# Kernel tuning notes

Hardware: AMD Instinct MI355X
Metric: run time of the kernel (lower is better)

## Reference

```python
import jax, jax.numpy as jnp
import numpy as np

NEG_SLOPE = 0.1  # negative slope of LeakyReLU in Conv3dReLU/Conv2dReLU


def setup_inputs() -> dict:
    key = jax.random.key(0)
    ks = jax.random.split(key, 16)
    B, C, PREV, N, M1, M2 = 2, 16, 16, 16384, 4096, 4096
    D1, CORR, FILT = 4, 15, 15          # d1 = d+1; (r+1)^d1 - r^d1 with r=1
    CO0, CO1 = 32, 32                    # num_corr_output
    O0, O1 = 64, 64                      # num_output
    CIN = 2 * C + PREV                   # corr_conv input channels

    feat1 = jax.random.normal(ks[0], (B, C, M1), jnp.float32)
    feat2 = jax.random.normal(ks[1], (B, C, M2), jnp.float32)
    prev_corr_feat = jax.random.normal(ks[2], (B, PREV, N), jnp.float32)
    barycentric1 = jax.random.uniform(ks[3], (B, D1, N), jnp.float32)
    # lattice_offset1: batch-offset flattened indices into [0, B*(M1+1)); value -1+1=0 is the pad slot
    local = jax.random.randint(ks[4], (B, D1, N), 0, M1)
    lattice_offset1 = local + (jnp.arange(B, dtype=jnp.int64) * (M1 + 1))[:, None, None]
    pc1_corr_indices = jax.random.randint(ks[5], (B, CORR, M1), -1, M1).astype(jnp.int64)
    pc2_corr_indices = jax.random.randint(ks[6], (B, FILT, CORR, M1), -1, M2).astype(jnp.int64)

    s = 0.05
    cw0 = jax.random.normal(ks[7], (CO0, CIN, CORR), jnp.float32) * s   # Conv3d (1,corr_size,1)
    cb0 = jax.random.normal(ks[8], (CO0,), jnp.float32) * s
    cw1 = jax.random.normal(ks[9], (CO1, CO0), jnp.float32) * s        # Conv3d 1x1x1
    cb1 = jax.random.normal(ks[10], (CO1,), jnp.float32) * s
    bw0 = jax.random.normal(ks[11], (O0, CO1, FILT), jnp.float32) * s  # Conv2d (filter_size,1)
    bb0 = jax.random.normal(ks[12], (O0,), jnp.float32) * s
    bw1 = jax.random.normal(ks[13], (O1, O0), jnp.float32) * s         # Conv2d 1x1 (no relu)
    bb1 = jax.random.normal(ks[14], (O1,), jnp.float32) * s

    return {
        "feat1": feat1, "feat2": feat2, "prev_corr_feat": prev_corr_feat,
        "barycentric1": barycentric1,
        "cw0": cw0, "cb0": cb0, "cw1": cw1, "cb1": cb1,
        "bw0": bw0, "bb0": bb0, "bw1": bw1, "bb1": bb1,
        "lattice_offset1": lattice_offset1,
        "pc1_corr_indices": pc1_corr_indices,
        "pc2_corr_indices": pc2_corr_indices,
        "max_hash_cnt1": M1, "max_hash_cnt2": M2,
    }


def reference(feat1, feat2, prev_corr_feat, barycentric1,
              cw0, cb0, cw1, cb1, bw0, bb0, bw1, bb1,
              lattice_offset1, pc1_corr_indices, pc2_corr_indices,
              max_hash_cnt1, max_hash_cnt2):
    B, C, M1 = feat1.shape
    PREV = prev_corr_feat.shape[1]

    # ---- splat prev_corr_feat onto lattice vertices (scatter-add) ----
    flat_idx = (lattice_offset1 + 1).reshape(-1)                      # (B*d1*N,)
    # (B, PREV, d1, N) -> (B, d1, N, PREV) -> (B*d1*N, PREV)
    vals = (barycentric1[:, None, :, :] * prev_corr_feat[:, :, None, :])
    vals = vals.transpose(0, 2, 3, 1).reshape(-1, PREV)
    prev_splat = jax.ops.segment_sum(vals, flat_idx, num_segments=B * (M1 + 1))
    prev_splat = prev_splat.reshape(B, M1 + 1, PREV).transpose(0, 2, 1)  # (B, PREV, M1+1)

    # use_norm: normalize by splatted barycentric mass
    ones_splat = jax.ops.segment_sum(barycentric1.reshape(-1), flat_idx,
                                     num_segments=B * (M1 + 1)).reshape(B, M1 + 1)
    prev_splat = prev_splat * (1.0 / (ones_splat + 1e-5))[:, None, :]

    # ---- prepend zero pad slot (index 0 catches -1 neighbor indices) ----
    splat1 = jnp.concatenate([prev_splat, jnp.pad(feat1, ((0, 0), (0, 0), (1, 0)))], axis=1)  # (B, PREV+C, M1+1)
    splat2 = jnp.pad(feat2, ((0, 0), (0, 0), (1, 0)))                                          # (B, C, M2+1)

    # ---- irregular gathers ----
    g1 = jax.vmap(lambda s, i: s[:, i])(splat1, pc1_corr_indices + 1)   # (B, PREV+C, corr, M1)
    g2 = jax.vmap(lambda s, i: s[:, i])(splat2, pc2_corr_indices + 1)   # (B, C, filt, corr, M1)
    FILT = g2.shape[2]
    g1b = jnp.broadcast_to(g1[:, :, None], (B, g1.shape[1], FILT, g1.shape[2], M1))
    combined = jnp.concatenate([g1b, g2], axis=1)                       # (B, 2C+PREV, filt, corr, M1)

    # ---- corr_conv: Conv3d(1,corr,1)+LeakyReLU, then 1x1x1+LeakyReLU ----
    x = jnp.einsum('bifkn,oik->bofn', combined, cw0) + cb0[None, :, None, None]
    x = jax.nn.leaky_relu(x, NEG_SLOPE)
    x = jnp.einsum('bcfn,oc->bofn', x, cw1) + cb1[None, :, None, None]
    x = jax.nn.leaky_relu(x, NEG_SLOPE)

    # ---- blur_conv: Conv2d(filt,1)+LeakyReLU, then 1x1 (last_relu=False) ----
    y = jnp.einsum('bcfn,ocf->bon', x, bw0) + bb0[None, :, None]
    y = jax.nn.leaky_relu(y, NEG_SLOPE)
    y = jnp.einsum('bcn,oc->bon', y, bw1) + bb1[None, :, None]
    return y
```

## Files before the change

### kernel.cpp

```cpp
#include <hip/hip_runtime.h>
#include <hip/hip_bf16.h>

namespace {

constexpr int B     = 2;
constexpr int C     = 16;
constexpr int PREVC = 16;
constexpr int NPTS  = 16384;
constexpr int M1    = 4096;
constexpr int D1    = 4;
constexpr int CORR  = 15;
constexpr int FILT  = 15;
constexpr int CIN   = 48;
constexpr int CO0   = 32;
constexpr int O1    = 64;
constexpr int MS    = M1 + 1;
constexpr int NSLOT = B * MS;
constexpr int NPAIR = B * D1 * NPTS;
constexpr int BCAP  = 64;
constexpr int GSTR  = 240;
constexpr float NEG = 0.1f;

constexpr size_t OFF_SP1   = 0;
constexpr size_t SZ_SP1    = (size_t)NSLOT * 32;
constexpr size_t OFF_SP2   = OFF_SP1 + SZ_SP1;
constexpr size_t SZ_SP2    = (size_t)NSLOT * 16;
constexpr size_t OFF_P     = OFF_SP2 + SZ_SP2;
constexpr size_t SZ_PQ     = (size_t)B * CORR * MS * 32 / 2;
constexpr size_t OFF_Q     = OFF_P + SZ_PQ;
constexpr size_t OFF_CWT   = OFF_Q + SZ_PQ;
constexpr size_t SZ_CWT    = (size_t)CORR * CIN * 32;
constexpr size_t OFF_W0R   = OFF_CWT + SZ_CWT;
constexpr size_t SZ_W0R    = 512 * 64;
constexpr size_t OFF_H     = OFF_W0R + SZ_W0R;
constexpr size_t SZ_H      = (size_t)B * M1 * 512 / 2;
constexpr size_t OFF_PREVT = OFF_H + SZ_H;
constexpr size_t SZ_PREVT  = (size_t)B * NPTS * 16;
constexpr size_t OFF_CNT   = OFF_PREVT + SZ_PREVT;
constexpr size_t SZ_CNT    = 8208;
constexpr size_t OFF_REC   = OFF_CNT + SZ_CNT;
constexpr size_t SZ_REC    = (size_t)NSLOT * BCAP;
constexpr size_t OFF_GT    = OFF_REC + SZ_REC;
constexpr size_t SZ_GT     = (size_t)B * M1 * GSTR / 2;

__device__ __forceinline__ float leaky(float v) { return v > 0.f ? v : NEG * v; }
__device__ __forceinline__ float bflo(unsigned u) { return __uint_as_float(u << 16); }
__device__ __forceinline__ float bfhi(unsigned u) { return __uint_as_float(u & 0xffff0000u); }

__global__ __launch_bounds__(256) void k_pre(const int* __restrict__ lo,
                                             const float* __restrict__ prev,
                                             const float* __restrict__ cw0,
                                             const float* __restrict__ bw0,
                                             const int* __restrict__ pc1,
                                             const int* __restrict__ pc2,
                                             int* __restrict__ counts,
                                             int* __restrict__ rec,
                                             float* __restrict__ prevT,
                                             float* __restrict__ cwT,
                                             float* __restrict__ W0r,
                                             unsigned short* __restrict__ gT) {
  int bx = blockIdx.x, tid = threadIdx.x;
  if (bx < 512) {
    int t = bx * 256 + tid;
    int slot = lo[t] + 1;
    int pos = atomicAdd(counts + slot, 1);
    if (pos < BCAP) rec[slot * BCAP + pos] = t;
  } else if (bx < 1024) {
    __shared__ float tile[16][65];
    int bb = bx - 512;
    int b = bb >> 8, n0 = (bb & 255) * 64;
    for (int e = tid; e < 1024; e += 256) {
      int ln = e & 63, r = e >> 6;
      tile[r][ln] = prev[((size_t)b * PREVC + r) * NPTS + n0 + ln];
    }
    __syncthreads();
    for (int e = tid; e < 1024; e += 256) {
      int c = e & 15, nn = e >> 4;
      prevT[((size_t)b * NPTS + n0 + nn) * 16 + c] = tile[c][nn];
    }
  } else if (bx < 1243) {
    int e = (bx - 1024) * 256 + tid;
    if (e < CORR * CIN * 32) {
      int o = e & 31, i = (e >> 5) % CIN, k = e / (CIN * 32);
      cwT[e] = cw0[((size_t)o * CIN + i) * CORR + k];
    }
    int e2 = e - CORR * CIN * 32;
    if (e2 >= 0 && e2 < 512 * 64) {
      int o3 = e2 & 63, cf = e2 >> 6, c = cf >> 4, f = cf & 15;
      W0r[e2] = (f < FILT) ? bw0[((size_t)o3 * CO0 + c) * FILT + f] : 0.f;
    }
  } else {
    __shared__ int tile[16][65];
    int t = bx - 1243;
    int n0 = (t & 63) * 64;
    int rest = t >> 6;
    int b = rest & 1;
    int rt = rest >> 1;
    const int* src; int r0, nr, doff;
    if (rt < 15) { src = pc2 + (size_t)b * FILT * CORR * M1; r0 = rt * 16;
                   nr = min(16, FILT * CORR - r0); doff = 0; }
    else         { src = pc1 + (size_t)b * CORR * M1; r0 = 0; nr = CORR; doff = 225; }
    for (int e = tid; e < nr * 64; e += 256) {
      int ln = e & 63, r = e >> 6;
      tile[r][ln] = src[(size_t)(r0 + r) * M1 + n0 + ln] + 1;
    }
    __syncthreads();
    for (int e = tid; e < 1024; e += 256) {
      int rr = e & 15, nn = e >> 4;
      if (rr < nr)
        gT[((size_t)b * M1 + n0 + nn) * GSTR + doff + r0 + rr] =
            (unsigned short)tile[rr][nn];
    }
  }
}

__global__ __launch_bounds__(256) void k_sum(const int* __restrict__ rec,
                                             const int* __restrict__ counts,
                                             const float* __restrict__ bary,
                                             const float* __restrict__ prevT,
                                             const float* __restrict__ feat1,
                                             const float* __restrict__ feat2,
                                             float* __restrict__ splat1,
                                             float* __restrict__ splat2) {
  int tid = threadIdx.x;
  int s = blockIdx.x * 4 + (tid >> 6);
  if (s >= NSLOT) return;
  int lane = tid & 63, c = lane & 15, g = lane >> 4;
  int cnt = min(counts[s], BCAP);
  const int* bucket = rec + (size_t)s * BCAP;
  float acc = 0.f, wsum = 0.f;
  for (int e = g; e < cnt; e += 4) {
    int t = bucket[e];
    float w = bary[t];
    int n = t & (NPTS - 1);
    int b = t >> 16;
    acc += w * prevT[((size_t)b * NPTS + n) * 16 + c];
    wsum += w;
  }
  acc  += __shfl_down(acc, 32);  acc  += __shfl_down(acc, 16);
  wsum += __shfl_down(wsum, 32); wsum += __shfl_down(wsum, 16);
  if (lane < 16) {
    int m = s % MS, b2 = s / MS;
    float scale = 1.f / (wsum + 1e-5f);
    splat1[(size_t)s * 32 + c] = acc * scale;
    float f1 = (m == 0) ? 0.f : feat1[((size_t)b2 * C + c) * M1 + (m - 1)];
    splat1[(size_t)s * 32 + 16 + c] = f1;
    float f2 = (m == 0) ? 0.f : feat2[((size_t)b2 * C + c) * M1 + (m - 1)];
    splat2[(size_t)s * 16 + c] = f2;
  }
}

__global__ __launch_bounds__(256) void k_pq(const float* __restrict__ sp1,
                                            const float* __restrict__ sp2,
                                            const float* __restrict__ cwT,
                                            __hip_bfloat16* __restrict__ Pt,
                                            __hip_bfloat16* __restrict__ Qt) {
  __shared__ float wk[CIN][33];
  int k = blockIdx.y, b = blockIdx.z;
  int tid = threadIdx.x;
  int m = blockIdx.x * 16 + (tid >> 4);
  int o2 = tid & 15;
  for (int e = tid; e < CIN * 32; e += 256)
    wk[e >> 5][e & 31] = cwT[(size_t)k * CIN * 32 + e];
  __syncthreads();
  if (m >= MS) return;
  const float* s1 = sp1 + ((size_t)b * MS + m) * 32;
  const float* s2 = sp2 + ((size_t)b * MS + m) * 16;
  int oa = o2 * 2, ob = oa + 1;
  float q0 = 0, q1 = 0, p0 = 0, p1 = 0;
#pragma unroll
  for (int i4 = 0; i4 < 8; ++i4) {
    float4 s = *(const float4*)(s1 + i4 * 4);
    q0 += s.x * wk[i4*4+0][oa] + s.y * wk[i4*4+1][oa] + s.z * wk[i4*4+2][oa] + s.w * wk[i4*4+3][oa];
    q1 += s.x * wk[i4*4+0][ob] + s.y * wk[i4*4+1][ob] + s.z * wk[i4*4+2][ob] + s.w * wk[i4*4+3][ob];
  }
#pragma unroll
  for (int i4 = 0; i4 < 4; ++i4) {
    float4 s = *(const float4*)(s2 + i4 * 4);
    p0 += s.x * wk[32+i4*4+0][oa] + s.y * wk[32+i4*4+1][oa] + s.z * wk[32+i4*4+2][oa] + s.w * wk[32+i4*4+3][oa];
    p1 += s.x * wk[32+i4*4+0][ob] + s.y * wk[32+i4*4+1][ob] + s.z * wk[32+i4*4+2][ob] + s.w * wk[32+i4*4+3][ob];
  }
  size_t base = ((size_t)(b * CORR + k) * MS + m) * 32;
  __hip_bfloat162 qq, pp;
  qq.x = __float2bfloat16(q0); qq.y = __float2bfloat16(q1);
  pp.x = __float2bfloat16(p0); pp.y = __float2bfloat16(p1);
  *reinterpret_cast<__hip_bfloat162*>(Qt + base + oa) = qq;
  *reinterpret_cast<__hip_bfloat162*>(Pt + base + oa) = pp;
}

__global__ __launch_bounds__(256) void k_gather(const __hip_bfloat16* __restrict__ Pt,
                                                const __hip_bfloat16* __restrict__ Qt,
                                                const unsigned short* __restrict__ gT,
                                                const float* __restrict__ cw1,
                                                const float* __restrict__ cb0,
                                                const float* __restrict__ cb1,
                                                __hip_bfloat16* __restrict__ hbuf) {
  __shared__ unsigned short idxs[4][GSTR];
  __shared__ float p1s[4][32];
  __shared__ float xls[4][16][33];

  int bid = blockIdx.x;
  int b = (bid >> 2) & 1;
  int r = bid & 3, x = bid >> 3;
  int n0 = (r << 10) | (x << 2);
  int pt0 = (b << 12) | n0;
  int tid = threadIdx.x;

  for (int e = tid; e < 480; e += 256) {
    int pl = e / 120, d = e - pl * 120;
    ((unsigned int*)idxs[pl])[d] =
        ((const unsigned int*)(gT + (size_t)(pt0 + pl) * GSTR))[d];
  }
  __syncthreads();

  int pl = tid >> 6, lane = tid & 63;
  int f = lane >> 2, o4 = lane & 3;

  {
    const __hip_bfloat16* base = (f < CORR ? Pt : Qt) + (size_t)b * CORR * MS * 32;
    const unsigned short* ip = &idxs[pl][f < CORR ? f * CORR : 225];
    float a[8] = {};
#pragma unroll
    for (int k = 0; k < CORR; ++k) {
      unsigned int idx = ip[k];
      uint4 d = *(const uint4*)(base + ((size_t)k * MS + idx) * 32 + o4 * 8);
      a[0] += bflo(d.x); a[1] += bfhi(d.x);
      a[2] += bflo(d.y); a[3] += bfhi(d.y);
      a[4] += bflo(d.z); a[5] += bfhi(d.z);
      a[6] += bflo(d.w); a[7] += bfhi(d.w);
    }
    if (f == CORR) {
#pragma unroll
      for (int j = 0; j < 8; ++j)
        p1s[pl][o4 * 8 + j] = a[j] + cb0[o4 * 8 + j];
    }
    __syncthreads();
    if (f < CORR) {
#pragma unroll
      for (int j = 0; j < 8; ++j)
        xls[pl][f][o4 * 8 + j] = leaky(a[j] + p1s[pl][o4 * 8 + j]);
    }
  }
  __syncthreads();

  {
    int o = lane & 31, fh = lane >> 5;
    const float* wrow = cw1 + o * CO0;
    float bias = cb1[o];
    float h[8];
#pragma unroll
    for (int j = 0; j < 8; ++j) {
      float hh = bias;
#pragma unroll
      for (int c4 = 0; c4 < 8; ++c4) {
        float4 xv = *(const float4*)&xls[pl][fh * 8 + j][c4 * 4];
        float4 w  = *(const float4*)(wrow + c4 * 4);
        hh += w.x * xv.x + w.y * xv.y + w.z * xv.z + w.w * xv.w;
      }
      h[j] = leaky(hh);
    }
    if (fh == 1) h[7] = 0.f;
    union { __hip_bfloat16 hb[8]; uint4 u; } pk;
#pragma unroll
    for (int j = 0; j < 8; ++j) pk.hb[j] = __float2bfloat16(h[j]);
    *(uint4*)(hbuf + (size_t)(pt0 + pl) * 512 + o * 16 + fh * 8) = pk.u;
  }
}

__global__ __launch_bounds__(256) void k_blur(const __hip_bfloat16* __restrict__ hbuf,
                                              const float* __restrict__ W0r,
                                              const float* __restrict__ bb0,
                                              const float* __restrict__ bw1,
                                              const float* __restrict__ bb1,
                                              float* __restrict__ out) {
  __shared__ float hs[64][33];
  __shared__ float ws[64][68];
  __shared__ float y0s[64][36];

  int bid = blockIdx.x;
  int b = bid >> 7;
  int n0 = (bid & 127) * 32;
  int tid = threadIdx.x;
  int og = tid & 15, ng = tid >> 4;

  float acc[4][2] = {};
  for (int kc = 0; kc < 512; kc += 64) {
    __syncthreads();
    {
      int nn = tid >> 3, k8 = tid & 7;
      const __hip_bfloat16* hp = hbuf + ((size_t)b * M1 + n0 + nn) * 512 + kc + k8 * 8;
#pragma unroll
      for (int j = 0; j < 4; ++j) {
        __hip_bfloat162 v2 = *(const __hip_bfloat162*)(hp + j * 2);
        hs[k8 * 8 + j * 2 + 0][nn] = __bfloat162float(v2.x);
        hs[k8 * 8 + j * 2 + 1][nn] = __bfloat162float(v2.y);
      }
    }
    for (int e = tid; e < 1024; e += 256) {
      int row = e >> 4, c4 = e & 15;
      *(float4*)&ws[row][c4 * 4] = *(const float4*)(W0r + (size_t)(kc + row) * 64 + c4 * 4);
    }
    __syncthreads();
#pragma unroll 16
    for (int kk = 0; kk < 64; ++kk) {
      float4 w = *(const float4*)&ws[kk][og * 4];
      float h0 = hs[kk][ng * 2], h1 = hs[kk][ng * 2 + 1];
      acc[0][0] += w.x * h0; acc[0][1] += w.x * h1;
      acc[1][0] += w.y * h0; acc[1][1] += w.y * h1;
      acc[2][0] += w.z * h0; acc[2][1] += w.z * h1;
      acc[3][0] += w.w * h0; acc[3][1] += w.w * h1;
    }
  }
  __syncthreads();

#pragma unroll
  for (int i = 0; i < 4; ++i) {
    int o3 = og * 4 + i;
    float bias = bb0[o3];
#pragma unroll
    for (int j = 0; j < 2; ++j)
      y0s[o3][ng * 2 + j] = leaky(acc[i][j] + bias);
  }
  for (int e = tid; e < 64 * 64; e += 256) {
    int o1e = e >> 6, c = e & 63;
    ws[c][o1e] = bw1[e];
  }
  __syncthreads();

  int o1 = tid & 63, ng4 = tid >> 6;
  float a8[8] = {};
  for (int c = 0; c < 64; ++c) {
    float w = ws[c][o1];
    float4 ya = *(const float4*)&y0s[c][ng4 * 8];
    float4 yb = *(const float4*)&y0s[c][ng4 * 8 + 4];
    a8[0] += w * ya.x; a8[1] += w * ya.y; a8[2] += w * ya.z; a8[3] += w * ya.w;
    a8[4] += w * yb.x; a8[5] += w * yb.y; a8[6] += w * yb.z; a8[7] += w * yb.w;
  }
  float bias = bb1[o1];
#pragma unroll
  for (int j = 0; j < 8; ++j)
    out[((size_t)b * O1 + o1) * M1 + n0 + ng4 * 8 + j] = a8[j] + bias;
}

}

extern "C" void kernel_launch(void* const* d_in, const int* in_sizes, int n_in,
                              void* d_out, int out_size, void* d_ws, size_t ws_size,
                              hipStream_t stream) {
  const float* feat1 = (const float*)d_in[0];
  const float* feat2 = (const float*)d_in[1];
  const float* prev  = (const float*)d_in[2];
  const float* bary  = (const float*)d_in[3];
  const float* cw0   = (const float*)d_in[4];
  const float* cb0   = (const float*)d_in[5];
  const float* cw1   = (const float*)d_in[6];
  const float* cb1   = (const float*)d_in[7];
  const float* bw0   = (const float*)d_in[8];
  const float* bb0   = (const float*)d_in[9];
  const float* bw1   = (const float*)d_in[10];
  const float* bb1   = (const float*)d_in[11];
  const int* lo  = (const int*)d_in[12];
  const int* pc1 = (const int*)d_in[13];
  const int* pc2 = (const int*)d_in[14];

  float* ws = (float*)d_ws;
  float* splat1 = ws + OFF_SP1;
  float* splat2 = ws + OFF_SP2;
  __hip_bfloat16* Pt = (__hip_bfloat16*)(ws + OFF_P);
  __hip_bfloat16* Qt = (__hip_bfloat16*)(ws + OFF_Q);
  float* cwT   = ws + OFF_CWT;
  float* W0r   = ws + OFF_W0R;
  __hip_bfloat16* hbuf = (__hip_bfloat16*)(ws + OFF_H);
  float* prevT = ws + OFF_PREVT;
  int* counts  = (int*)(ws + OFF_CNT);
  int* rec     = (int*)(ws + OFF_REC);
  unsigned short* gT = (unsigned short*)(ws + OFF_GT);
  float* out   = (float*)d_out;

  hipMemsetAsync(counts, 0, NSLOT * sizeof(int), stream);

  hipLaunchKernelGGL(k_pre, dim3(1243 + 2048), dim3(256), 0, stream,
                     lo, prev, cw0, bw0, pc1, pc2, counts, rec, prevT, cwT, W0r, gT);
  hipLaunchKernelGGL(k_sum, dim3((NSLOT + 3) / 4), dim3(256), 0, stream,
                     rec, counts, bary, prevT, feat1, feat2, splat1, splat2);
  hipLaunchKernelGGL(k_pq, dim3((MS + 15) / 16, CORR, B), dim3(256), 0, stream,
                     splat1, splat2, cwT, Pt, Qt);
  hipLaunchKernelGGL(k_gather, dim3(B * M1 / 4), dim3(256), 0, stream,
                     Pt, Qt, gT, cw1, cb0, cb1, hbuf);
  hipLaunchKernelGGL(k_blur, dim3(B * M1 / 32), dim3(256), 0, stream,
                     hbuf, W0r, bb0, bw1, bb1, out);
}
```

Baseline: 124.8 us.

## Loop k_pq over corr taps in-block with shared splat rows; barrier-step gather loads

New measurement: 146.7 us. +17.5%, slower.

```diff
diff --git a/kernel.cpp b/kernel.cpp
--- a/kernel.cpp
+++ b/kernel.cpp
@@ -155,37 +155,49 @@
                                             const float* __restrict__ cwT,
                                             __hip_bfloat16* __restrict__ Pt,
                                             __hip_bfloat16* __restrict__ Qt) {
+  __shared__ float s1s[16][33];
+  __shared__ float s2s[16][17];
   __shared__ float wk[CIN][33];
-  int k = blockIdx.y, b = blockIdx.z;
+  int b = blockIdx.y;
   int tid = threadIdx.x;
-  int m = blockIdx.x * 16 + (tid >> 4);
-  int o2 = tid & 15;
-  for (int e = tid; e < CIN * 32; e += 256)
-    wk[e >> 5][e & 31] = cwT[(size_t)k * CIN * 32 + e];
-  __syncthreads();
-  if (m >= MS) return;
-  const float* s1 = sp1 + ((size_t)b * MS + m) * 32;
-  const float* s2 = sp2 + ((size_t)b * MS + m) * 16;
+  int m0 = blockIdx.x * 16;
+  int mm = tid >> 4, o2 = tid & 15;
+  int m = m0 + mm;
+  for (int e = tid; e < 512; e += 256) {
+    int r = e >> 5, i = e & 31;
+    s1s[r][i] = (m0 + r < MS) ? sp1[((size_t)b * MS + m0 + r) * 32 + i] : 0.f;
+  }
+  {
+    int r = tid >> 4, i = tid & 15;
+    s2s[r][i] = (m0 + r < MS) ? sp2[((size_t)b * MS + m0 + r) * 16 + i] : 0.f;
+  }
+  bool valid = (m < MS);
   int oa = o2 * 2, ob = oa + 1;
-  float q0 = 0, q1 = 0, p0 = 0, p1 = 0;
-#pragma unroll
-  for (int i4 = 0; i4 < 8; ++i4) {
-    float4 s = *(const float4*)(s1 + i4 * 4);
-    q0 += s.x * wk[i4*4+0][oa] + s.y * wk[i4*4+1][oa] + s.z * wk[i4*4+2][oa] + s.w * wk[i4*4+3][oa];
-    q1 += s.x * wk[i4*4+0][ob] + s.y * wk[i4*4+1][ob] + s.z * wk[i4*4+2][ob] + s.w * wk[i4*4+3][ob];
-  }
-#pragma unroll
-  for (int i4 = 0; i4 < 4; ++i4) {
-    float4 s = *(const float4*)(s2 + i4 * 4);
-    p0 += s.x * wk[32+i4*4+0][oa] + s.y * wk[32+i4*4+1][oa] + s.z * wk[32+i4*4+2][oa] + s.w * wk[32+i4*4+3][oa];
-    p1 += s.x * wk[32+i4*4+0][ob] + s.y * wk[32+i4*4+1][ob] + s.z * wk[32+i4*4+2][ob] + s.w * wk[32+i4*4+3][ob];
-  }
-  size_t base = ((size_t)(b * CORR + k) * MS + m) * 32;
-  __hip_bfloat162 qq, pp;
-  qq.x = __float2bfloat16(q0); qq.y = __float2bfloat16(q1);
-  pp.x = __float2bfloat16(p0); pp.y = __float2bfloat16(p1);
-  *reinterpret_cast<__hip_bfloat162*>(Qt + base + oa) = qq;
-  *reinterpret_cast<__hip_bfloat162*>(Pt + base + oa) = pp;
+  for (int k = 0; k < CORR; ++k) {
+    __syncthreads();
+    for (int e = tid; e < CIN * 32; e += 256)
+      wk[e >> 5][e & 31] = cwT[(size_t)k * CIN * 32 + e];
+    __syncthreads();
+    if (valid) {
+      float q0 = 0, q1 = 0, p0 = 0, p1 = 0;
+#pragma unroll
+      for (int i = 0; i < 32; ++i) {
+        float s = s1s[mm][i];
+        q0 += s * wk[i][oa]; q1 += s * wk[i][ob];
+      }
+#pragma unroll
+      for (int i = 0; i < 16; ++i) {
+        float s = s2s[mm][i];
+        p0 += s * wk[32 + i][oa]; p1 += s * wk[32 + i][ob];
+      }
+      size_t base = ((size_t)(b * CORR + k) * MS + m) * 32;
+      __hip_bfloat162 qq, pp;
+      qq.x = __float2bfloat16(q0); qq.y = __float2bfloat16(q1);
+      pp.x = __float2bfloat16(p0); pp.y = __float2bfloat16(p1);
+      *reinterpret_cast<__hip_bfloat162*>(Qt + base + oa) = qq;
+      *reinterpret_cast<__hip_bfloat162*>(Pt + base + oa) = pp;
+    }
+  }
 }
 
 __global__ __launch_bounds__(256) void k_gather(const __hip_bfloat16* __restrict__ Pt,
@@ -216,12 +228,14 @@
   int pl = tid >> 6, lane = tid & 63;
   int f = lane >> 2, o4 = lane & 3;
 
-  {
-    const __hip_bfloat16* base = (f < CORR ? Pt : Qt) + (size_t)b * CORR * MS * 32;
-    const unsigned short* ip = &idxs[pl][f < CORR ? f * CORR : 225];
-    float a[8] = {};
-#pragma unroll
-    for (int k = 0; k < CORR; ++k) {
+  const __hip_bfloat16* base = (f < CORR ? Pt : Qt) + (size_t)b * CORR * MS * 32;
+  const unsigned short* ip = &idxs[pl][f < CORR ? f * CORR : 225];
+  float a[8] = {};
+#pragma unroll
+  for (int kw = 0; kw < 3; ++kw) {
+#pragma unroll
+    for (int kk = 0; kk < 5; ++kk) {
+      int k = kw * 5 + kk;
       unsigned int idx = ip[k];
       uint4 d = *(const uint4*)(base + ((size_t)k * MS + idx) * 32 + o4 * 8);
       a[0] += bflo(d.x); a[1] += bfhi(d.x);
@@ -229,17 +243,18 @@
       a[4] += bflo(d.z); a[5] += bfhi(d.z);
       a[6] += bflo(d.w); a[7] += bfhi(d.w);
     }
-    if (f == CORR) {
-#pragma unroll
-      for (int j = 0; j < 8; ++j)
-        p1s[pl][o4 * 8 + j] = a[j] + cb0[o4 * 8 + j];
-    }
-    __syncthreads();
-    if (f < CORR) {
-#pragma unroll
-      for (int j = 0; j < 8; ++j)
-        xls[pl][f][o4 * 8 + j] = leaky(a[j] + p1s[pl][o4 * 8 + j]);
-    }
+    __syncthreads();
+  }
+  if (f == CORR) {
+#pragma unroll
+    for (int j = 0; j < 8; ++j)
+      p1s[pl][o4 * 8 + j] = a[j] + cb0[o4 * 8 + j];
+  }
+  __syncthreads();
+  if (f < CORR) {
+#pragma unroll
+    for (int j = 0; j < 8; ++j)
+      xls[pl][f][o4 * 8 + j] = leaky(a[j] + p1s[pl][o4 * 8 + j]);
   }
   __syncthreads();
 
@@ -383,7 +398,7 @@
                      lo, prev, cw0, bw0, pc1, pc2, counts, rec, prevT, cwT, W0r, gT);
   hipLaunchKernelGGL(k_sum, dim3((NSLOT + 3) / 4), dim3(256), 0, stream,
                      rec, counts, bary, prevT, feat1, feat2, splat1, splat2);
-  hipLaunchKernelGGL(k_pq, dim3((MS + 15) / 16, CORR, B), dim3(256), 0, stream,
+  hipLaunchKernelGGL(k_pq, dim3((MS + 15) / 16, B), dim3(256), 0, stream,
                      splat1, splat2, cwT, Pt, Qt);
   hipLaunchKernelGGL(k_gather, dim3(B * M1 / 4), dim3(256), 0, stream,
                      Pt, Qt, gT, cw1, cb0, cb1, hbuf);
```
